# Kernel tuning notes

Measured on AMD Instinct MI355X. Metric: run time of the kernel, lower is better.

The kernel has to match this reference:

```python
import jax, jax.numpy as jnp
import numpy as np

B, C, L = 4, 256, 2048
HEADS, DIM_HEAD = 8, 64
HIDDEN = HEADS * DIM_HEAD  # 512


def setup_inputs() -> dict:
    key = jax.random.key(0)
    k1, k2, k3, k4 = jax.random.split(key, 4)
    x = jax.random.normal(k1, (B, C, L), dtype=jnp.float32)
    # Conv1d kernel_size=1 weights, squeezed to [out_ch, in_ch]
    w_qkv = jax.random.normal(k2, (3 * HIDDEN, C), dtype=jnp.float32) * (1.0 / np.sqrt(C))
    w_out = jax.random.normal(k3, (C, HIDDEN), dtype=jnp.float32) * (1.0 / np.sqrt(HIDDEN))
    b_out = jax.random.normal(k4, (C,), dtype=jnp.float32) * 0.01
    return {"x": x, "w_qkv": w_qkv, "w_out": w_out, "b_out": b_out}


def reference(x, w_qkv, w_out, b_out):
    b, c, l = x.shape
    scale = DIM_HEAD ** (-0.5)
    # pointwise conv == channel matmul
    qkv = jnp.einsum('oc,bcl->bol', w_qkv, x)  # [b, 3*hidden, l]
    q, k, v = jnp.split(qkv, 3, axis=1)        # each [b, hidden, l]
    def to_heads(t):
        return t.reshape(b, HEADS, DIM_HEAD, l)  # b h d l
    q, k, v = to_heads(q), to_heads(k), to_heads(v)
    q = q * scale
    sim = jnp.einsum('bhdi,bhdj->bhij', q, k)   # [b,h,l,l]
    attn = jax.nn.softmax(sim, axis=-1)          # stable softmax (max-subtract inside)
    out = jnp.einsum('bhij,bhdj->bhid', attn, v)  # [b,h,l,d]
    out = out.transpose(0, 1, 3, 2).reshape(b, HIDDEN, l)  # b (h d) l
    return jnp.einsum('oc,bcl->bol', w_out, out) + b_out[None, :, None]
```

## Files before the change

kernel.cpp:

```cpp
#include <hip/hip_runtime.h>

typedef unsigned short u16;
typedef unsigned int u32;
typedef __bf16 bf16x8 __attribute__((ext_vector_type(8)));
typedef float f32x4 __attribute__((ext_vector_type(4)));
typedef float f32x8 __attribute__((ext_vector_type(8)));
typedef float f32x16 __attribute__((ext_vector_type(16)));

#define MFMA16(a, b, c) __builtin_amdgcn_mfma_f32_16x16x32_bf16((a), (b), (c), 0, 0, 0)
#define MFMA32(a, b, c) __builtin_amdgcn_mfma_f32_32x32x16_bf16((a), (b), (c), 0, 0, 0)

#define Bn 4
#define Cn 256
#define Ln 2048
#define Hn 8
#define Dn 64
#define HID 512
#define SEGELEMS 4194304

__device__ __forceinline__ u16 bf16_rne(float f) {
  u32 u = __builtin_bit_cast(u32, f);
  u += 0x7FFFu + ((u >> 16) & 1u);
  return (u16)(u >> 16);
}

__device__ __forceinline__ unsigned pack2(float a, float b) {
  return (unsigned)bf16_rne(a) | ((unsigned)bf16_rne(b) << 16);
}

__device__ __forceinline__ float bf16_up(u16 v) {
  u32 u = ((u32)v) << 16;
  return __builtin_bit_cast(float, u);
}

__device__ __forceinline__ float fast_exp2(float x) {
#if __has_builtin(__builtin_amdgcn_exp2f)
  return __builtin_amdgcn_exp2f(x);
#else
  return exp2f(x);
#endif
}

__device__ __forceinline__ float fast_rcp(float x) {
#if __has_builtin(__builtin_amdgcn_rcpf)
  return __builtin_amdgcn_rcpf(x);
#else
  return 1.0f / x;
#endif
}

__device__ __forceinline__ void async_load16(const u16* g, u16* l) {
  __builtin_amdgcn_global_load_lds(
      (const __attribute__((address_space(1))) void*)g,
      (__attribute__((address_space(3))) void*)l, 16, 0, 0);
}

__global__ __launch_bounds__(256) void prep_all(const float* __restrict__ wqkv,
                                                const float* __restrict__ wout,
                                                const float* __restrict__ x,
                                                u16* __restrict__ wq,
                                                u16* __restrict__ wo,
                                                u16* __restrict__ xT) {
  const int t = threadIdx.x;
  if (blockIdx.x < 2048) {
    int i = blockIdx.x * 256 + t;
    const float QSCALE = 0.125f * 1.44269504088896340736f;
    if (i < 3 * HID * Cn) {
      float v = wqkv[i];
      if (i < HID * Cn) v *= QSCALE;
      wq[i] = bf16_rne(v);
    } else {
      int j = i - 3 * HID * Cn;
      wo[j] = bf16_rne(wout[j]);
    }
    return;
  }
  __shared__ u16 tile[64][72];
  int v = blockIdx.x - 2048;
  const int lt = v & 31, ct = (v >> 5) & 3, b = v >> 7;
  const float* xp = x + ((size_t)b * Cn + ct * 64) * Ln + lt * 64;
  for (int pass = 0; pass < 4; ++pass) {
    int c = pass * 16 + (t >> 4);
    int l4 = (t & 15) * 4;
    float4 vf = *(const float4*)(xp + (size_t)c * Ln + l4);
    tile[l4 + 0][c] = bf16_rne(vf.x);
    tile[l4 + 1][c] = bf16_rne(vf.y);
    tile[l4 + 2][c] = bf16_rne(vf.z);
    tile[l4 + 3][c] = bf16_rne(vf.w);
  }
  __syncthreads();
  u16* op = xT + ((size_t)b * Ln + lt * 64) * Cn + ct * 64;
  for (int pass = 0; pass < 2; ++pass) {
    int id = pass * 256 + t;
    int l = id >> 3, c8 = (id & 7) * 8;
    *(uint4*)(op + (size_t)l * Cn + c8) = *(const uint4*)&tile[l][c8];
  }
}

__global__ __launch_bounds__(256, 4) void qkv_gemm(const u16* __restrict__ wq,
                                                   const u16* __restrict__ xT,
                                                   u16* __restrict__ qT,
                                                   u16* __restrict__ kT,
                                                   u16* __restrict__ vv) {
  __shared__ u16 Bs[4096];
  __shared__ u16 Aq[4096];
  __shared__ u16 Ak[4096];
  __shared__ u16 Av[4096];
  const int t = threadIdx.x;
  const int nt = blockIdx.x, head = blockIdx.y, b = blockIdx.z;
  const int n0 = nt * 64, m0 = head * 64;
  const int w = t >> 6, lane = t & 63, q = lane >> 4, ln = lane & 15;

  const u16* Bg = xT + ((size_t)b * Ln + n0) * Cn;
  const u16* AgQ = wq + (size_t)m0 * Cn;
  const u16* AgK = wq + (size_t)(512 + m0) * Cn;
  const u16* AgV = wq + (size_t)(1024 + m0) * Cn;

  f32x4 zf = {0.f, 0.f, 0.f, 0.f};
  f32x4 accQ[4], accK[4], accV[4];
  for (int i = 0; i < 4; ++i) { accQ[i] = zf; accK[i] = zf; accV[i] = zf; }

  const int pr0 = w * 8 + (lane >> 3), pr1 = (4 + w) * 8 + (lane >> 3);
  const int pc0 = (lane & 7) ^ (pr0 & 7), pc1 = (lane & 7) ^ (pr1 & 7);

  for (int kk = 0; kk < 4; ++kk) {
    int k0 = kk * 64;
    async_load16(Bg + (size_t)pr0 * Cn + k0 + pc0 * 8, &Bs[w * 512]);
    async_load16(Bg + (size_t)pr1 * Cn + k0 + pc1 * 8, &Bs[(4 + w) * 512]);
    async_load16(AgQ + (size_t)pr0 * Cn + k0 + pc0 * 8, &Aq[w * 512]);
    async_load16(AgQ + (size_t)pr1 * Cn + k0 + pc1 * 8, &Aq[(4 + w) * 512]);
    async_load16(AgK + (size_t)pr0 * Cn + k0 + pc0 * 8, &Ak[w * 512]);
    async_load16(AgK + (size_t)pr1 * Cn + k0 + pc1 * 8, &Ak[(4 + w) * 512]);
    async_load16(AgV + (size_t)pr0 * Cn + k0 + pc0 * 8, &Av[w * 512]);
    async_load16(AgV + (size_t)pr1 * Cn + k0 + pc1 * 8, &Av[(4 + w) * 512]);
    __syncthreads();
    int ar = w * 16 + ln;
    bf16x8 aq0 = *(const bf16x8*)&Aq[ar * 64 + ((q ^ (ln & 7)) * 8)];
    bf16x8 aq1 = *(const bf16x8*)&Aq[ar * 64 + (((q + 4) ^ (ln & 7)) * 8)];
    bf16x8 ak0 = *(const bf16x8*)&Ak[ar * 64 + ((q ^ (ln & 7)) * 8)];
    bf16x8 ak1 = *(const bf16x8*)&Ak[ar * 64 + (((q + 4) ^ (ln & 7)) * 8)];
    bf16x8 av0 = *(const bf16x8*)&Av[ar * 64 + ((q ^ (ln & 7)) * 8)];
    bf16x8 av1 = *(const bf16x8*)&Av[ar * 64 + (((q + 4) ^ (ln & 7)) * 8)];
    for (int n2 = 0; n2 < 4; ++n2) {
      int br = n2 * 16 + ln;
      bf16x8 b0 = *(const bf16x8*)&Bs[br * 64 + ((q ^ (ln & 7)) * 8)];
      bf16x8 b1 = *(const bf16x8*)&Bs[br * 64 + (((q + 4) ^ (ln & 7)) * 8)];
      accQ[n2] = MFMA16(aq0, b0, accQ[n2]);
      accQ[n2] = MFMA16(aq1, b1, accQ[n2]);
      accK[n2] = MFMA16(ak0, b0, accK[n2]);
      accK[n2] = MFMA16(ak1, b1, accK[n2]);
      accV[n2] = MFMA16(av0, b0, accV[n2]);
      accV[n2] = MFMA16(av1, b1, accV[n2]);
    }
    __syncthreads();
  }

  int od0 = w * 16 + q * 4;
  int cw = od0 >> 3, lo = od0 & 7;
  for (int n2 = 0; n2 < 4; ++n2) {
    int l = n2 * 16 + ln;
    uint2 pk;
    pk.x = pack2(accQ[n2][0], accQ[n2][1]);
    pk.y = pack2(accQ[n2][2], accQ[n2][3]);
    *(uint2*)&Bs[l * 64 + ((cw ^ (l & 7)) * 8) + lo] = pk;
  }
  __syncthreads();
  {
    u16* dst = qT + (((size_t)b * Hn + head) * Ln + n0) * Dn;
    for (int pass = 0; pass < 2; ++pass) {
      int id = pass * 256 + t;
      int l = id >> 3, c = id & 7;
      *(uint4*)(dst + (size_t)l * Dn + c * 8) =
          *(const uint4*)&Bs[l * 64 + ((c ^ (l & 7)) * 8)];
    }
  }
  __syncthreads();
  for (int n2 = 0; n2 < 4; ++n2) {
    int l = n2 * 16 + ln;
    uint2 pk;
    pk.x = pack2(accK[n2][0], accK[n2][1]);
    pk.y = pack2(accK[n2][2], accK[n2][3]);
    *(uint2*)&Bs[l * 64 + ((cw ^ (l & 7)) * 8) + lo] = pk;
  }
  __syncthreads();
  {
    u16* dst = kT + (((size_t)b * Hn + head) * Ln + n0) * Dn;
    for (int pass = 0; pass < 2; ++pass) {
      int id = pass * 256 + t;
      int l = id >> 3, c = id & 7;
      *(uint4*)(dst + (size_t)l * Dn + c * 8) =
          *(const uint4*)&Bs[l * 64 + ((c ^ (l & 7)) * 8)];
    }
  }
  __syncthreads();
  for (int n2 = 0; n2 < 4; ++n2) {
    int l = n2 * 16 + ln;
    int lpm = (l & ~12) | ((l & 4) << 1) | ((l & 8) >> 1);
    int cl = lpm >> 3, lov = lpm & 7;
    for (int r = 0; r < 4; ++r) {
      int od = w * 16 + q * 4 + r;
      Bs[od * 64 + ((cl ^ (od & 7)) * 8) + lov] = bf16_rne(accV[n2][r]);
    }
  }
  __syncthreads();
  {
    u16* dst = vv + ((size_t)b * HID + head * 64) * Ln + n0;
    for (int pass = 0; pass < 2; ++pass) {
      int id = pass * 256 + t;
      int od = id >> 3, c = id & 7;
      *(uint4*)(dst + (size_t)od * Ln + c * 8) =
          *(const uint4*)&Bs[od * 64 + ((c ^ (od & 7)) * 8)];
    }
  }
}

__global__ __launch_bounds__(256, 4) void attention(const u16* __restrict__ qT,
                                                    const u16* __restrict__ kT,
                                                    const u16* __restrict__ vv,
                                                    u16* __restrict__ pO,
                                                    float* __restrict__ lP) {
  __shared__ u16 Kt[4096];
  __shared__ u16 Vt[4096];
  const int t = threadIdx.x;
  const int qb = blockIdx.x, bh = blockIdx.y, seg = blockIdx.z;
  const int b = bh >> 3, hh = bh & 7;
  const int w = t >> 6, lane = t & 63;
  const int li = lane & 31, h = lane >> 5;
  const int i0 = qb * 128 + w * 32;

  bf16x8 qf0, qf1, qf2, qf3;
  {
    const u16* qrow = qT + (((size_t)bh) * Ln + i0 + li) * Dn + h * 8;
    qf0 = *(const bf16x8*)(qrow + 0);
    qf1 = *(const bf16x8*)(qrow + 16);
    qf2 = *(const bf16x8*)(qrow + 32);
    qf3 = *(const bf16x8*)(qrow + 48);
  }

  const u16* ksrc0 = kT + ((size_t)bh) * Ln * Dn;
  const u16* vsrc0 = vv + ((size_t)b * HID + hh * Dn) * Ln;

  f32x16 z16;
#pragma unroll
  for (int r = 0; r < 16; ++r) z16[r] = 0.f;
  f32x16 o0 = z16, o1 = z16;
  float lp = 0.f;

  const int pr0 = w * 8 + (lane >> 3), pr1 = (4 + w) * 8 + (lane >> 3);
  const int pc0 = (lane & 7) ^ (pr0 & 7), pc1 = (lane & 7) ^ (pr1 & 7);
  const u16* kadr0 = ksrc0 + ((size_t)seg * 1024 + pr0) * Dn + pc0 * 8;
  const u16* kadr1 = ksrc0 + ((size_t)seg * 1024 + pr1) * Dn + pc1 * 8;
  const u16* vadr0 = vsrc0 + (size_t)pr0 * Ln + seg * 1024 + pc0 * 8;
  const u16* vadr1 = vsrc0 + (size_t)pr1 * Ln + seg * 1024 + pc1 * 8;

  const int sw = (li & 7);

  for (int jt = 0; jt < 16; ++jt) {
    int j0 = jt * 64;
    async_load16(kadr0 + (size_t)j0 * Dn, &Kt[w * 512]);
    async_load16(kadr1 + (size_t)j0 * Dn, &Kt[(4 + w) * 512]);
    async_load16(vadr0 + j0, &Vt[w * 512]);
    async_load16(vadr1 + j0, &Vt[(4 + w) * 512]);
    __syncthreads();

    f32x16 sv0, sv1;
    {
      bf16x8 k0 = *(const bf16x8*)&Kt[li * 64 + (((0 + h) ^ sw) * 8)];
      bf16x8 k1 = *(const bf16x8*)&Kt[(32 + li) * 64 + (((0 + h) ^ sw) * 8)];
      sv0 = MFMA32(k0, qf0, z16);
      sv1 = MFMA32(k1, qf0, z16);
    }
    {
      bf16x8 k0 = *(const bf16x8*)&Kt[li * 64 + (((2 + h) ^ sw) * 8)];
      bf16x8 k1 = *(const bf16x8*)&Kt[(32 + li) * 64 + (((2 + h) ^ sw) * 8)];
      sv0 = MFMA32(k0, qf1, sv0);
      sv1 = MFMA32(k1, qf1, sv1);
    }
    {
      bf16x8 k0 = *(const bf16x8*)&Kt[li * 64 + (((4 + h) ^ sw) * 8)];
      bf16x8 k1 = *(const bf16x8*)&Kt[(32 + li) * 64 + (((4 + h) ^ sw) * 8)];
      sv0 = MFMA32(k0, qf2, sv0);
      sv1 = MFMA32(k1, qf2, sv1);
    }
    {
      bf16x8 k0 = *(const bf16x8*)&Kt[li * 64 + (((6 + h) ^ sw) * 8)];
      bf16x8 k1 = *(const bf16x8*)&Kt[(32 + li) * 64 + (((6 + h) ^ sw) * 8)];
      sv0 = MFMA32(k0, qf3, sv0);
      sv1 = MFMA32(k1, qf3, sv1);
    }

#pragma unroll
    for (int g = 0; g < 16; ++g) {
      sv0[g] = fast_exp2(sv0[g]);
      sv1[g] = fast_exp2(sv1[g]);
      lp += sv0[g] + sv1[g];
    }
    f32x8 e0 = __builtin_shufflevector(sv0, sv0, 0, 1, 2, 3, 4, 5, 6, 7);
    f32x8 e1 = __builtin_shufflevector(sv0, sv0, 8, 9, 10, 11, 12, 13, 14, 15);
    f32x8 e2 = __builtin_shufflevector(sv1, sv1, 0, 1, 2, 3, 4, 5, 6, 7);
    f32x8 e3 = __builtin_shufflevector(sv1, sv1, 8, 9, 10, 11, 12, 13, 14, 15);
    bf16x8 pf0 = __builtin_convertvector(e0, bf16x8);
    bf16x8 pf1 = __builtin_convertvector(e1, bf16x8);
    bf16x8 pf2 = __builtin_convertvector(e2, bf16x8);
    bf16x8 pf3 = __builtin_convertvector(e3, bf16x8);

#pragma unroll
    for (int jc = 0; jc < 4; ++jc) {
      int ch = 2 * jc + h;
      bf16x8 pf = (jc == 0) ? pf0 : (jc == 1) ? pf1 : (jc == 2) ? pf2 : pf3;
      bf16x8 vf0 = *(const bf16x8*)&Vt[li * 64 + ((ch ^ sw) * 8)];
      bf16x8 vf1 = *(const bf16x8*)&Vt[(32 + li) * 64 + ((ch ^ sw) * 8)];
      o0 = MFMA32(pf, vf0, o0);
      o1 = MFMA32(pf, vf1, o1);
    }
    __syncthreads();
  }

  float lsum = lp + __shfl_xor(lp, 32);
  if (h == 0)
    lP[(((size_t)seg * Bn + b) * Hn + hh) * Ln + i0 + li] = lsum;
  u16* po = pO + (size_t)seg * SEGELEMS;
#pragma unroll
  for (int r = 0; r < 16; ++r) {
    int ir = (r & 3) + 8 * (r >> 2) + 4 * h;
    size_t base = ((size_t)b * Ln + i0 + ir) * HID + hh * Dn + li;
    po[base] = bf16_rne(o0[r]);
    po[base + 32] = bf16_rne(o1[r]);
  }
}

__global__ __launch_bounds__(256) void combine(const u16* __restrict__ pO,
                                               const float* __restrict__ lP,
                                               u16* __restrict__ attT) {
  int idx8 = (blockIdx.x * 256 + threadIdx.x) * 8;
  int i_lin = idx8 >> 9;
  int h = (idx8 & 511) >> 6;
  int b = i_lin >> 11, i = i_lin & 2047;
  float l = lP[(b * 8 + h) * 2048 + i] + lP[(32 + b * 8 + h) * 2048 + i];
  float s = fast_rcp(l);
  uint4 u0 = *(const uint4*)(pO + idx8);
  uint4 u1 = *(const uint4*)(pO + SEGELEMS + idx8);
  u32 a[4] = {u0.x, u0.y, u0.z, u0.w};
  u32 c[4] = {u1.x, u1.y, u1.z, u1.w};
  uint4 r;
  u32 rw[4];
#pragma unroll
  for (int k = 0; k < 4; ++k) {
    float flo = (bf16_up((u16)(a[k] & 0xFFFF)) + bf16_up((u16)(c[k] & 0xFFFF))) * s;
    float fhi = (bf16_up((u16)(a[k] >> 16)) + bf16_up((u16)(c[k] >> 16))) * s;
    rw[k] = pack2(flo, fhi);
  }
  r.x = rw[0]; r.y = rw[1]; r.z = rw[2]; r.w = rw[3];
  *(uint4*)(attT + idx8) = r;
}

__global__ __launch_bounds__(256, 4) void out_gemm(const u16* __restrict__ wo,
                                                   const u16* __restrict__ attT,
                                                   const float* __restrict__ bout,
                                                   float* __restrict__ out) {
  __shared__ u16 As[4096];
  __shared__ u16 Bs[2048];
  const int t = threadIdx.x;
  const int nt = blockIdx.x, mt = blockIdx.y, b = blockIdx.z;
  const int m0 = mt * 64, n0 = nt * 32;
  const int w = t >> 6, lane = t & 63, q = lane >> 4, ln = lane & 15;

  const u16* Ag = wo + (size_t)m0 * HID;
  const u16* Bg = attT + ((size_t)b * Ln + n0) * HID;

  f32x4 zf = {0.f, 0.f, 0.f, 0.f};
  f32x4 acc[2];
  acc[0] = zf; acc[1] = zf;

  const int pr0 = w * 8 + (lane >> 3), pr1 = (4 + w) * 8 + (lane >> 3);
  const int pc0 = (lane & 7) ^ (pr0 & 7), pc1 = (lane & 7) ^ (pr1 & 7);
  const u16* Aad0 = Ag + (size_t)pr0 * HID + pc0 * 8;
  const u16* Aad1 = Ag + (size_t)pr1 * HID + pc1 * 8;
  const u16* Bad0 = Bg + (size_t)pr0 * HID + pc0 * 8;

#define LOADAB(kk, A0, A1, B0)                   \
  {                                              \
    int k0_ = (kk) * 64;                         \
    A0 = *(const uint4*)(Aad0 + k0_);            \
    A1 = *(const uint4*)(Aad1 + k0_);            \
    B0 = *(const uint4*)(Bad0 + k0_);            \
  }
#define STOREAB(A0, A1, B0)                      \
  {                                              \
    *(uint4*)&As[w * 512 + lane * 8] = A0;       \
    *(uint4*)&As[(4 + w) * 512 + lane * 8] = A1; \
    *(uint4*)&Bs[w * 512 + lane * 8] = B0;       \
  }
#define COMPUTEC()                                                             \
  {                                                                            \
    int ar = w * 16 + ln;                                                      \
    bf16x8 a0 = *(const bf16x8*)&As[ar * 64 + ((q ^ (ln & 7)) * 8)];           \
    bf16x8 a1 = *(const bf16x8*)&As[ar * 64 + (((q + 4) ^ (ln & 7)) * 8)];     \
    for (int n2 = 0; n2 < 2; ++n2) {                                           \
      int br = n2 * 16 + ln;                                                   \
      bf16x8 b0 = *(const bf16x8*)&Bs[br * 64 + ((q ^ (ln & 7)) * 8)];         \
      bf16x8 b1 = *(const bf16x8*)&Bs[br * 64 + (((q + 4) ^ (ln & 7)) * 8)];   \
      acc[n2] = MFMA16(a0, b0, acc[n2]);                                       \
      acc[n2] = MFMA16(a1, b1, acc[n2]);                                       \
    }                                                                          \
  }

  uint4 aa0, aa1, ba0, ab0, ab1, bb0;
  LOADAB(0, aa0, aa1, ba0);
  for (int kk = 0; kk < 8; kk += 2) {
    if (kk) __syncthreads();
    STOREAB(aa0, aa1, ba0);
    __syncthreads();
    LOADAB(kk + 1, ab0, ab1, bb0);
    COMPUTEC();
    __syncthreads();
    STOREAB(ab0, ab1, bb0);
    __syncthreads();
    if (kk + 2 < 8) LOADAB(kk + 2, aa0, aa1, ba0);
    COMPUTEC();
  }
#undef LOADAB
#undef STOREAB
#undef COMPUTEC

  float bias[4];
  for (int r = 0; r < 4; ++r) bias[r] = bout[m0 + w * 16 + q * 4 + r];
  for (int n2 = 0; n2 < 2; ++n2) {
    int l = n0 + n2 * 16 + ln;
    for (int r = 0; r < 4; ++r) {
      int o = m0 + w * 16 + q * 4 + r;
      out[((size_t)b * Cn + o) * Ln + l] = acc[n2][r] + bias[r];
    }
  }
}

extern "C" void kernel_launch(void* const* d_in, const int* in_sizes, int n_in,
                              void* d_out, int out_size, void* d_ws, size_t ws_size,
                              hipStream_t stream) {
  const float* x = (const float*)d_in[0];
  const float* wqkv = (const float*)d_in[1];
  const float* wout = (const float*)d_in[2];
  const float* bout = (const float*)d_in[3];
  float* out = (float*)d_out;
  char* ws = (char*)d_ws;

  u16* wq_b  = (u16*)(ws + 0);
  u16* wo_b  = (u16*)(ws + 786432);
  float* lP  = (float*)(ws + 1048576);
  u16* qT    = (u16*)(ws + 1572864);
  u16* kT    = (u16*)(ws + 9961472);
  u16* vv    = (u16*)(ws + 18350080);
  u16* xT    = (u16*)(ws + 26738688);
  u16* pO    = (u16*)(ws + 26738688);
  u16* attT  = qT;

  prep_all<<<2560, 256, 0, stream>>>(wqkv, wout, x, wq_b, wo_b, xT);
  qkv_gemm<<<dim3(32, 8, 4), 256, 0, stream>>>(wq_b, xT, qT, kT, vv);
  attention<<<dim3(16, 32, 2), 256, 0, stream>>>(qT, kT, vv, pO, lP);
  combine<<<2048, 256, 0, stream>>>(pO, lP, attT);
  out_gemm<<<dim3(64, 4, 4), 256, 0, stream>>>(wo_b, attT, bout, out);
}
```

Before: 136.3 us.

## Fuse split-KV combine into output GEMM and register-prefetch K/V tiles

The separate combine kernel is removed. The output GEMM now loads both partial attention outputs and their row sums, normalizes them, and stages the result in shared memory. This saves a kernel launch and a full write and read of the intermediate attT tensor. In the attention loop, the async direct-to-LDS K/V loads are replaced with register double-buffered global loads followed by LDS stores, which costs more registers and changes the overlap pattern.

```diff
diff --git a/kernel.cpp b/kernel.cpp
--- a/kernel.cpp
+++ b/kernel.cpp
@@ -31,6 +31,12 @@
 __device__ __forceinline__ float bf16_up(u16 v) {
   u32 u = ((u32)v) << 16;
   return __builtin_bit_cast(float, u);
+}
+
+__device__ __forceinline__ u32 comb2(u32 a, u32 c, float s) {
+  float lo = (bf16_up((u16)(a & 0xFFFF)) + bf16_up((u16)(c & 0xFFFF))) * s;
+  float hi = (bf16_up((u16)(a >> 16)) + bf16_up((u16)(c >> 16))) * s;
+  return pack2(lo, hi);
 }
 
 __device__ __forceinline__ float fast_exp2(float x) {
@@ -255,66 +261,89 @@
 
   const int sw = (li & 7);
 
-  for (int jt = 0; jt < 16; ++jt) {
-    int j0 = jt * 64;
-    async_load16(kadr0 + (size_t)j0 * Dn, &Kt[w * 512]);
-    async_load16(kadr1 + (size_t)j0 * Dn, &Kt[(4 + w) * 512]);
-    async_load16(vadr0 + j0, &Vt[w * 512]);
-    async_load16(vadr1 + j0, &Vt[(4 + w) * 512]);
-    __syncthreads();
-
-    f32x16 sv0, sv1;
-    {
-      bf16x8 k0 = *(const bf16x8*)&Kt[li * 64 + (((0 + h) ^ sw) * 8)];
-      bf16x8 k1 = *(const bf16x8*)&Kt[(32 + li) * 64 + (((0 + h) ^ sw) * 8)];
-      sv0 = MFMA32(k0, qf0, z16);
-      sv1 = MFMA32(k1, qf0, z16);
-    }
-    {
-      bf16x8 k0 = *(const bf16x8*)&Kt[li * 64 + (((2 + h) ^ sw) * 8)];
-      bf16x8 k1 = *(const bf16x8*)&Kt[(32 + li) * 64 + (((2 + h) ^ sw) * 8)];
-      sv0 = MFMA32(k0, qf1, sv0);
-      sv1 = MFMA32(k1, qf1, sv1);
-    }
-    {
-      bf16x8 k0 = *(const bf16x8*)&Kt[li * 64 + (((4 + h) ^ sw) * 8)];
-      bf16x8 k1 = *(const bf16x8*)&Kt[(32 + li) * 64 + (((4 + h) ^ sw) * 8)];
-      sv0 = MFMA32(k0, qf2, sv0);
-      sv1 = MFMA32(k1, qf2, sv1);
-    }
-    {
-      bf16x8 k0 = *(const bf16x8*)&Kt[li * 64 + (((6 + h) ^ sw) * 8)];
-      bf16x8 k1 = *(const bf16x8*)&Kt[(32 + li) * 64 + (((6 + h) ^ sw) * 8)];
-      sv0 = MFMA32(k0, qf3, sv0);
-      sv1 = MFMA32(k1, qf3, sv1);
-    }
-
-#pragma unroll
-    for (int g = 0; g < 16; ++g) {
-      sv0[g] = fast_exp2(sv0[g]);
-      sv1[g] = fast_exp2(sv1[g]);
-      lp += sv0[g] + sv1[g];
-    }
-    f32x8 e0 = __builtin_shufflevector(sv0, sv0, 0, 1, 2, 3, 4, 5, 6, 7);
-    f32x8 e1 = __builtin_shufflevector(sv0, sv0, 8, 9, 10, 11, 12, 13, 14, 15);
-    f32x8 e2 = __builtin_shufflevector(sv1, sv1, 0, 1, 2, 3, 4, 5, 6, 7);
-    f32x8 e3 = __builtin_shufflevector(sv1, sv1, 8, 9, 10, 11, 12, 13, 14, 15);
-    bf16x8 pf0 = __builtin_convertvector(e0, bf16x8);
-    bf16x8 pf1 = __builtin_convertvector(e1, bf16x8);
-    bf16x8 pf2 = __builtin_convertvector(e2, bf16x8);
-    bf16x8 pf3 = __builtin_convertvector(e3, bf16x8);
-
-#pragma unroll
-    for (int jc = 0; jc < 4; ++jc) {
-      int ch = 2 * jc + h;
-      bf16x8 pf = (jc == 0) ? pf0 : (jc == 1) ? pf1 : (jc == 2) ? pf2 : pf3;
-      bf16x8 vf0 = *(const bf16x8*)&Vt[li * 64 + ((ch ^ sw) * 8)];
-      bf16x8 vf1 = *(const bf16x8*)&Vt[(32 + li) * 64 + ((ch ^ sw) * 8)];
-      o0 = MFMA32(pf, vf0, o0);
-      o1 = MFMA32(pf, vf1, o1);
-    }
-    __syncthreads();
-  }
+#define LOADKV(jt, K0, K1, V0, V1)                              \
+  {                                                             \
+    int j0_ = (jt) * 64;                                        \
+    K0 = *(const uint4*)(kadr0 + (size_t)j0_ * Dn);             \
+    K1 = *(const uint4*)(kadr1 + (size_t)j0_ * Dn);             \
+    V0 = *(const uint4*)(vadr0 + j0_);                          \
+    V1 = *(const uint4*)(vadr1 + j0_);                          \
+  }
+#define STOREKV(K0, K1, V0, V1)                                 \
+  {                                                             \
+    *(uint4*)&Kt[w * 512 + lane * 8] = K0;                      \
+    *(uint4*)&Kt[(4 + w) * 512 + lane * 8] = K1;                \
+    *(uint4*)&Vt[w * 512 + lane * 8] = V0;                      \
+    *(uint4*)&Vt[(4 + w) * 512 + lane * 8] = V1;                \
+  }
+
+#define COMPUTE()                                                              \
+  {                                                                            \
+    f32x16 sv0, sv1;                                                           \
+    {                                                                          \
+      bf16x8 k0 = *(const bf16x8*)&Kt[li * 64 + (((0 + h) ^ sw) * 8)];         \
+      bf16x8 k1 = *(const bf16x8*)&Kt[(32 + li) * 64 + (((0 + h) ^ sw) * 8)];  \
+      sv0 = MFMA32(k0, qf0, z16);                                              \
+      sv1 = MFMA32(k1, qf0, z16);                                              \
+    }                                                                          \
+    {                                                                          \
+      bf16x8 k0 = *(const bf16x8*)&Kt[li * 64 + (((2 + h) ^ sw) * 8)];         \
+      bf16x8 k1 = *(const bf16x8*)&Kt[(32 + li) * 64 + (((2 + h) ^ sw) * 8)];  \
+      sv0 = MFMA32(k0, qf1, sv0);                                              \
+      sv1 = MFMA32(k1, qf1, sv1);                                              \
+    }                                                                          \
+    {                                                                          \
+      bf16x8 k0 = *(const bf16x8*)&Kt[li * 64 + (((4 + h) ^ sw) * 8)];         \
+      bf16x8 k1 = *(const bf16x8*)&Kt[(32 + li) * 64 + (((4 + h) ^ sw) * 8)];  \
+      sv0 = MFMA32(k0, qf2, sv0);                                              \
+      sv1 = MFMA32(k1, qf2, sv1);                                              \
+    }                                                                          \
+    {                                                                          \
+      bf16x8 k0 = *(const bf16x8*)&Kt[li * 64 + (((6 + h) ^ sw) * 8)];         \
+      bf16x8 k1 = *(const bf16x8*)&Kt[(32 + li) * 64 + (((6 + h) ^ sw) * 8)];  \
+      sv0 = MFMA32(k0, qf3, sv0);                                              \
+      sv1 = MFMA32(k1, qf3, sv1);                                              \
+    }                                                                          \
+    _Pragma("unroll") for (int g = 0; g < 16; ++g) {                           \
+      sv0[g] = fast_exp2(sv0[g]);                                              \
+      sv1[g] = fast_exp2(sv1[g]);                                              \
+      lp += sv0[g] + sv1[g];                                                   \
+    }                                                                          \
+    f32x8 e0 = __builtin_shufflevector(sv0, sv0, 0, 1, 2, 3, 4, 5, 6, 7);      \
+    f32x8 e1 = __builtin_shufflevector(sv0, sv0, 8, 9, 10, 11, 12, 13, 14, 15);\
+    f32x8 e2 = __builtin_shufflevector(sv1, sv1, 0, 1, 2, 3, 4, 5, 6, 7);      \
+    f32x8 e3 = __builtin_shufflevector(sv1, sv1, 8, 9, 10, 11, 12, 13, 14, 15);\
+    bf16x8 pf0 = __builtin_convertvector(e0, bf16x8);                          \
+    bf16x8 pf1 = __builtin_convertvector(e1, bf16x8);                          \
+    bf16x8 pf2 = __builtin_convertvector(e2, bf16x8);                          \
+    bf16x8 pf3 = __builtin_convertvector(e3, bf16x8);                          \
+    _Pragma("unroll") for (int jc = 0; jc < 4; ++jc) {                         \
+      int ch = 2 * jc + h;                                                     \
+      bf16x8 pf = (jc == 0) ? pf0 : (jc == 1) ? pf1 : (jc == 2) ? pf2 : pf3;   \
+      bf16x8 vf0 = *(const bf16x8*)&Vt[li * 64 + ((ch ^ sw) * 8)];             \
+      bf16x8 vf1 = *(const bf16x8*)&Vt[(32 + li) * 64 + ((ch ^ sw) * 8)];      \
+      o0 = MFMA32(pf, vf0, o0);                                                \
+      o1 = MFMA32(pf, vf1, o1);                                                \
+    }                                                                          \
+  }
+
+  uint4 ka0, ka1, va0, va1, kb0, kb1, vb0, vb1;
+  LOADKV(0, ka0, ka1, va0, va1);
+  for (int jt = 0; jt < 16; jt += 2) {
+    if (jt) __syncthreads();
+    STOREKV(ka0, ka1, va0, va1);
+    __syncthreads();
+    LOADKV(jt + 1, kb0, kb1, vb0, vb1);
+    COMPUTE();
+    __syncthreads();
+    STOREKV(kb0, kb1, vb0, vb1);
+    __syncthreads();
+    if (jt + 2 < 16) LOADKV(jt + 2, ka0, ka1, va0, va1);
+    COMPUTE();
+  }
+#undef LOADKV
+#undef STOREKV
+#undef COMPUTE
 
   float lsum = lp + __shfl_xor(lp, 32);
   if (h == 0)
@@ -329,33 +358,9 @@
   }
 }
 
-__global__ __launch_bounds__(256) void combine(const u16* __restrict__ pO,
-                                               const float* __restrict__ lP,
-                                               u16* __restrict__ attT) {
-  int idx8 = (blockIdx.x * 256 + threadIdx.x) * 8;
-  int i_lin = idx8 >> 9;
-  int h = (idx8 & 511) >> 6;
-  int b = i_lin >> 11, i = i_lin & 2047;
-  float l = lP[(b * 8 + h) * 2048 + i] + lP[(32 + b * 8 + h) * 2048 + i];
-  float s = fast_rcp(l);
-  uint4 u0 = *(const uint4*)(pO + idx8);
-  uint4 u1 = *(const uint4*)(pO + SEGELEMS + idx8);
-  u32 a[4] = {u0.x, u0.y, u0.z, u0.w};
-  u32 c[4] = {u1.x, u1.y, u1.z, u1.w};
-  uint4 r;
-  u32 rw[4];
-#pragma unroll
-  for (int k = 0; k < 4; ++k) {
-    float flo = (bf16_up((u16)(a[k] & 0xFFFF)) + bf16_up((u16)(c[k] & 0xFFFF))) * s;
-    float fhi = (bf16_up((u16)(a[k] >> 16)) + bf16_up((u16)(c[k] >> 16))) * s;
-    rw[k] = pack2(flo, fhi);
-  }
-  r.x = rw[0]; r.y = rw[1]; r.z = rw[2]; r.w = rw[3];
-  *(uint4*)(attT + idx8) = r;
-}
-
 __global__ __launch_bounds__(256, 4) void out_gemm(const u16* __restrict__ wo,
-                                                   const u16* __restrict__ attT,
+                                                   const u16* __restrict__ pO,
+                                                   const float* __restrict__ lP,
                                                    const float* __restrict__ bout,
                                                    float* __restrict__ out) {
   __shared__ u16 As[4096];
@@ -366,7 +371,6 @@
   const int w = t >> 6, lane = t & 63, q = lane >> 4, ln = lane & 15;
 
   const u16* Ag = wo + (size_t)m0 * HID;
-  const u16* Bg = attT + ((size_t)b * Ln + n0) * HID;
 
   f32x4 zf = {0.f, 0.f, 0.f, 0.f};
   f32x4 acc[2];
@@ -376,20 +380,33 @@
   const int pc0 = (lane & 7) ^ (pr0 & 7), pc1 = (lane & 7) ^ (pr1 & 7);
   const u16* Aad0 = Ag + (size_t)pr0 * HID + pc0 * 8;
   const u16* Aad1 = Ag + (size_t)pr1 * HID + pc1 * 8;
-  const u16* Bad0 = Bg + (size_t)pr0 * HID + pc0 * 8;
-
-#define LOADAB(kk, A0, A1, B0)                   \
+  const int irow = n0 + pr0;
+  const u16* Bs0 = pO + ((size_t)b * Ln + irow) * HID + pc0 * 8;
+  const u16* Bs1 = Bs0 + SEGELEMS;
+  const float* lp0 = lP + (size_t)b * Hn * Ln + irow;
+  const float* lp1 = lP + (size_t)(Bn + b) * Hn * Ln + irow;
+
+#define LOADAB(kk, A0, A1, U0, U1, L0, L1)       \
   {                                              \
     int k0_ = (kk) * 64;                         \
     A0 = *(const uint4*)(Aad0 + k0_);            \
     A1 = *(const uint4*)(Aad1 + k0_);            \
-    B0 = *(const uint4*)(Bad0 + k0_);            \
-  }
-#define STOREAB(A0, A1, B0)                      \
+    U0 = *(const uint4*)(Bs0 + k0_);             \
+    U1 = *(const uint4*)(Bs1 + k0_);             \
+    L0 = lp0[(size_t)(kk) * Ln];                 \
+    L1 = lp1[(size_t)(kk) * Ln];                 \
+  }
+#define STOREAB(A0, A1, U0, U1, L0, L1)          \
   {                                              \
+    float s_ = fast_rcp(L0 + L1);                \
+    uint4 Bc_;                                   \
+    Bc_.x = comb2(U0.x, U1.x, s_);               \
+    Bc_.y = comb2(U0.y, U1.y, s_);               \
+    Bc_.z = comb2(U0.z, U1.z, s_);               \
+    Bc_.w = comb2(U0.w, U1.w, s_);               \
     *(uint4*)&As[w * 512 + lane * 8] = A0;       \
     *(uint4*)&As[(4 + w) * 512 + lane * 8] = A1; \
-    *(uint4*)&Bs[w * 512 + lane * 8] = B0;       \
+    *(uint4*)&Bs[w * 512 + lane * 8] = Bc_;      \
   }
 #define COMPUTEC()                                                             \
   {                                                                            \
@@ -405,18 +422,19 @@
     }                                                                          \
   }
 
-  uint4 aa0, aa1, ba0, ab0, ab1, bb0;
-  LOADAB(0, aa0, aa1, ba0);
+  uint4 aa0, aa1, ua0, ua1, ab0, ab1, ub0, ub1;
+  float la0, la1, lb0, lb1;
+  LOADAB(0, aa0, aa1, ua0, ua1, la0, la1);
   for (int kk = 0; kk < 8; kk += 2) {
     if (kk) __syncthreads();
-    STOREAB(aa0, aa1, ba0);
-    __syncthreads();
-    LOADAB(kk + 1, ab0, ab1, bb0);
+    STOREAB(aa0, aa1, ua0, ua1, la0, la1);
+    __syncthreads();
+    LOADAB(kk + 1, ab0, ab1, ub0, ub1, lb0, lb1);
     COMPUTEC();
     __syncthreads();
-    STOREAB(ab0, ab1, bb0);
-    __syncthreads();
-    if (kk + 2 < 8) LOADAB(kk + 2, aa0, aa1, ba0);
+    STOREAB(ab0, ab1, ub0, ub1, lb0, lb1);
+    __syncthreads();
+    if (kk + 2 < 8) LOADAB(kk + 2, aa0, aa1, ua0, ua1, la0, la1);
     COMPUTEC();
   }
 #undef LOADAB
@@ -452,11 +470,9 @@
   u16* vv    = (u16*)(ws + 18350080);
   u16* xT    = (u16*)(ws + 26738688);
   u16* pO    = (u16*)(ws + 26738688);
-  u16* attT  = qT;
 
   prep_all<<<2560, 256, 0, stream>>>(wqkv, wout, x, wq_b, wo_b, xT);
   qkv_gemm<<<dim3(32, 8, 4), 256, 0, stream>>>(wq_b, xT, qT, kT, vv);
   attention<<<dim3(16, 32, 2), 256, 0, stream>>>(qT, kT, vv, pO, lP);
-  combine<<<2048, 256, 0, stream>>>(pO, lP, attT);
-  out_gemm<<<dim3(64, 4, 4), 256, 0, stream>>>(wo_b, attT, bout, out);
-}
+  out_gemm<<<dim3(64, 4, 4), 256, 0, stream>>>(wo_b, pO, lP, bout, out);
+}
```

Result: slower. 164.3 us (+20.6%).

## Fuse split-K combine into out_gemm and give attention waves two query tiles

Applied to the files above, without the earlier changes.

The separate combine kernel is removed. out_gemm now loads both partial attention outputs and their row sums, normalises them and writes the combined bf16 tile into shared memory before the MFMA loop, which saves one launch and one global round trip of the attention tensor. The attention kernel moves to 128-thread blocks in which each wave handles 64 query rows (two 32-row tiles), so every K/V fragment read from LDS feeds twice as many MFMAs. In exchange, register pressure per wave rises and each block has half as many waves to hide latency.

```diff
diff --git a/kernel.cpp b/kernel.cpp
--- a/kernel.cpp
+++ b/kernel.cpp
@@ -31,6 +31,12 @@
 __device__ __forceinline__ float bf16_up(u16 v) {
   u32 u = ((u32)v) << 16;
   return __builtin_bit_cast(float, u);
+}
+
+__device__ __forceinline__ u32 comb2(u32 a, u32 c, float s) {
+  float lo = (bf16_up((u16)(a & 0xFFFF)) + bf16_up((u16)(c & 0xFFFF))) * s;
+  float hi = (bf16_up((u16)(a >> 16)) + bf16_up((u16)(c >> 16))) * s;
+  return pack2(lo, hi);
 }
 
 __device__ __forceinline__ float fast_exp2(float x) {
@@ -214,7 +220,7 @@
   }
 }
 
-__global__ __launch_bounds__(256, 4) void attention(const u16* __restrict__ qT,
+__global__ __launch_bounds__(128, 2) void attention(const u16* __restrict__ qT,
                                                     const u16* __restrict__ kT,
                                                     const u16* __restrict__ vv,
                                                     u16* __restrict__ pO,
@@ -226,15 +232,20 @@
   const int b = bh >> 3, hh = bh & 7;
   const int w = t >> 6, lane = t & 63;
   const int li = lane & 31, h = lane >> 5;
-  const int i0 = qb * 128 + w * 32;
-
-  bf16x8 qf0, qf1, qf2, qf3;
+  const int i0 = qb * 128 + w * 64;
+
+  bf16x8 qA0, qA1, qA2, qA3, qB0, qB1, qB2, qB3;
   {
-    const u16* qrow = qT + (((size_t)bh) * Ln + i0 + li) * Dn + h * 8;
-    qf0 = *(const bf16x8*)(qrow + 0);
-    qf1 = *(const bf16x8*)(qrow + 16);
-    qf2 = *(const bf16x8*)(qrow + 32);
-    qf3 = *(const bf16x8*)(qrow + 48);
+    const u16* qra = qT + (((size_t)bh) * Ln + i0 + li) * Dn + h * 8;
+    const u16* qrb = qT + (((size_t)bh) * Ln + i0 + 32 + li) * Dn + h * 8;
+    qA0 = *(const bf16x8*)(qra + 0);
+    qA1 = *(const bf16x8*)(qra + 16);
+    qA2 = *(const bf16x8*)(qra + 32);
+    qA3 = *(const bf16x8*)(qra + 48);
+    qB0 = *(const bf16x8*)(qrb + 0);
+    qB1 = *(const bf16x8*)(qrb + 16);
+    qB2 = *(const bf16x8*)(qrb + 32);
+    qB3 = *(const bf16x8*)(qrb + 48);
   }
 
   const u16* ksrc0 = kT + ((size_t)bh) * Ln * Dn;
@@ -243,119 +254,136 @@
   f32x16 z16;
 #pragma unroll
   for (int r = 0; r < 16; ++r) z16[r] = 0.f;
-  f32x16 o0 = z16, o1 = z16;
-  float lp = 0.f;
-
-  const int pr0 = w * 8 + (lane >> 3), pr1 = (4 + w) * 8 + (lane >> 3);
-  const int pc0 = (lane & 7) ^ (pr0 & 7), pc1 = (lane & 7) ^ (pr1 & 7);
-  const u16* kadr0 = ksrc0 + ((size_t)seg * 1024 + pr0) * Dn + pc0 * 8;
-  const u16* kadr1 = ksrc0 + ((size_t)seg * 1024 + pr1) * Dn + pc1 * 8;
-  const u16* vadr0 = vsrc0 + (size_t)pr0 * Ln + seg * 1024 + pc0 * 8;
-  const u16* vadr1 = vsrc0 + (size_t)pr1 * Ln + seg * 1024 + pc1 * 8;
-
-  const int sw = (li & 7);
+  f32x16 oA0 = z16, oA1 = z16, oB0 = z16, oB1 = z16;
+  float lpA = 0.f, lpB = 0.f;
+
+  const int sr0 = (0 * 2 + w) * 8 + (lane >> 3);
+  const int sr1 = (1 * 2 + w) * 8 + (lane >> 3);
+  const int sr2 = (2 * 2 + w) * 8 + (lane >> 3);
+  const int sr3 = (3 * 2 + w) * 8 + (lane >> 3);
+  const int sc0 = (lane & 7) ^ (sr0 & 7), sc1 = (lane & 7) ^ (sr1 & 7);
+  const int sc2 = (lane & 7) ^ (sr2 & 7), sc3 = (lane & 7) ^ (sr3 & 7);
+  const u16* ka0 = ksrc0 + ((size_t)seg * 1024 + sr0) * Dn + sc0 * 8;
+  const u16* ka1 = ksrc0 + ((size_t)seg * 1024 + sr1) * Dn + sc1 * 8;
+  const u16* ka2 = ksrc0 + ((size_t)seg * 1024 + sr2) * Dn + sc2 * 8;
+  const u16* ka3 = ksrc0 + ((size_t)seg * 1024 + sr3) * Dn + sc3 * 8;
+  const u16* va0 = vsrc0 + (size_t)sr0 * Ln + seg * 1024 + sc0 * 8;
+  const u16* va1 = vsrc0 + (size_t)sr1 * Ln + seg * 1024 + sc1 * 8;
+  const u16* va2 = vsrc0 + (size_t)sr2 * Ln + seg * 1024 + sc2 * 8;
+  const u16* va3 = vsrc0 + (size_t)sr3 * Ln + seg * 1024 + sc3 * 8;
+
+  const int sw = li & 7;
 
   for (int jt = 0; jt < 16; ++jt) {
     int j0 = jt * 64;
-    async_load16(kadr0 + (size_t)j0 * Dn, &Kt[w * 512]);
-    async_load16(kadr1 + (size_t)j0 * Dn, &Kt[(4 + w) * 512]);
-    async_load16(vadr0 + j0, &Vt[w * 512]);
-    async_load16(vadr1 + j0, &Vt[(4 + w) * 512]);
-    __syncthreads();
-
-    f32x16 sv0, sv1;
+    async_load16(ka0 + (size_t)j0 * Dn, &Kt[(0 * 2 + w) * 512]);
+    async_load16(ka1 + (size_t)j0 * Dn, &Kt[(1 * 2 + w) * 512]);
+    async_load16(ka2 + (size_t)j0 * Dn, &Kt[(2 * 2 + w) * 512]);
+    async_load16(ka3 + (size_t)j0 * Dn, &Kt[(3 * 2 + w) * 512]);
+    async_load16(va0 + j0, &Vt[(0 * 2 + w) * 512]);
+    async_load16(va1 + j0, &Vt[(1 * 2 + w) * 512]);
+    async_load16(va2 + j0, &Vt[(2 * 2 + w) * 512]);
+    async_load16(va3 + j0, &Vt[(3 * 2 + w) * 512]);
+    __syncthreads();
+
+    f32x16 svA0, svA1, svB0, svB1;
     {
       bf16x8 k0 = *(const bf16x8*)&Kt[li * 64 + (((0 + h) ^ sw) * 8)];
       bf16x8 k1 = *(const bf16x8*)&Kt[(32 + li) * 64 + (((0 + h) ^ sw) * 8)];
-      sv0 = MFMA32(k0, qf0, z16);
-      sv1 = MFMA32(k1, qf0, z16);
+      svA0 = MFMA32(k0, qA0, z16);
+      svA1 = MFMA32(k1, qA0, z16);
+      svB0 = MFMA32(k0, qB0, z16);
+      svB1 = MFMA32(k1, qB0, z16);
     }
     {
       bf16x8 k0 = *(const bf16x8*)&Kt[li * 64 + (((2 + h) ^ sw) * 8)];
       bf16x8 k1 = *(const bf16x8*)&Kt[(32 + li) * 64 + (((2 + h) ^ sw) * 8)];
-      sv0 = MFMA32(k0, qf1, sv0);
-      sv1 = MFMA32(k1, qf1, sv1);
+      svA0 = MFMA32(k0, qA1, svA0);
+      svA1 = MFMA32(k1, qA1, svA1);
+      svB0 = MFMA32(k0, qB1, svB0);
+      svB1 = MFMA32(k1, qB1, svB1);
     }
     {
       bf16x8 k0 = *(const bf16x8*)&Kt[li * 64 + (((4 + h) ^ sw) * 8)];
       bf16x8 k1 = *(const bf16x8*)&Kt[(32 + li) * 64 + (((4 + h) ^ sw) * 8)];
-      sv0 = MFMA32(k0, qf2, sv0);
-      sv1 = MFMA32(k1, qf2, sv1);
+      svA0 = MFMA32(k0, qA2, svA0);
+      svA1 = MFMA32(k1, qA2, svA1);
+      svB0 = MFMA32(k0, qB2, svB0);
+      svB1 = MFMA32(k1, qB2, svB1);
     }
     {
       bf16x8 k0 = *(const bf16x8*)&Kt[li * 64 + (((6 + h) ^ sw) * 8)];
       bf16x8 k1 = *(const bf16x8*)&Kt[(32 + li) * 64 + (((6 + h) ^ sw) * 8)];
-      sv0 = MFMA32(k0, qf3, sv0);
-      sv1 = MFMA32(k1, qf3, sv1);
+      svA0 = MFMA32(k0, qA3, svA0);
+      svA1 = MFMA32(k1, qA3, svA1);
+      svB0 = MFMA32(k0, qB3, svB0);
+      svB1 = MFMA32(k1, qB3, svB1);
     }
 
 #pragma unroll
     for (int g = 0; g < 16; ++g) {
-      sv0[g] = fast_exp2(sv0[g]);
-      sv1[g] = fast_exp2(sv1[g]);
-      lp += sv0[g] + sv1[g];
-    }
-    f32x8 e0 = __builtin_shufflevector(sv0, sv0, 0, 1, 2, 3, 4, 5, 6, 7);
-    f32x8 e1 = __builtin_shufflevector(sv0, sv0, 8, 9, 10, 11, 12, 13, 14, 15);
-    f32x8 e2 = __builtin_shufflevector(sv1, sv1, 0, 1, 2, 3, 4, 5, 6, 7);
-    f32x8 e3 = __builtin_shufflevector(sv1, sv1, 8, 9, 10, 11, 12, 13, 14, 15);
-    bf16x8 pf0 = __builtin_convertvector(e0, bf16x8);
-    bf16x8 pf1 = __builtin_convertvector(e1, bf16x8);
-    bf16x8 pf2 = __builtin_convertvector(e2, bf16x8);
-    bf16x8 pf3 = __builtin_convertvector(e3, bf16x8);
+      svA0[g] = fast_exp2(svA0[g]);
+      svA1[g] = fast_exp2(svA1[g]);
+      lpA += svA0[g] + svA1[g];
+      svB0[g] = fast_exp2(svB0[g]);
+      svB1[g] = fast_exp2(svB1[g]);
+      lpB += svB0[g] + svB1[g];
+    }
+    bf16x8 pfA0 = __builtin_convertvector(
+        __builtin_shufflevector(svA0, svA0, 0, 1, 2, 3, 4, 5, 6, 7), bf16x8);
+    bf16x8 pfA1 = __builtin_convertvector(
+        __builtin_shufflevector(svA0, svA0, 8, 9, 10, 11, 12, 13, 14, 15), bf16x8);
+    bf16x8 pfA2 = __builtin_convertvector(
+        __builtin_shufflevector(svA1, svA1, 0, 1, 2, 3, 4, 5, 6, 7), bf16x8);
+    bf16x8 pfA3 = __builtin_convertvector(
+        __builtin_shufflevector(svA1, svA1, 8, 9, 10, 11, 12, 13, 14, 15), bf16x8);
+    bf16x8 pfB0 = __builtin_convertvector(
+        __builtin_shufflevector(svB0, svB0, 0, 1, 2, 3, 4, 5, 6, 7), bf16x8);
+    bf16x8 pfB1 = __builtin_convertvector(
+        __builtin_shufflevector(svB0, svB0, 8, 9, 10, 11, 12, 13, 14, 15), bf16x8);
+    bf16x8 pfB2 = __builtin_convertvector(
+        __builtin_shufflevector(svB1, svB1, 0, 1, 2, 3, 4, 5, 6, 7), bf16x8);
+    bf16x8 pfB3 = __builtin_convertvector(
+        __builtin_shufflevector(svB1, svB1, 8, 9, 10, 11, 12, 13, 14, 15), bf16x8);
 
 #pragma unroll
     for (int jc = 0; jc < 4; ++jc) {
       int ch = 2 * jc + h;
-      bf16x8 pf = (jc == 0) ? pf0 : (jc == 1) ? pf1 : (jc == 2) ? pf2 : pf3;
+      bf16x8 pa = (jc == 0) ? pfA0 : (jc == 1) ? pfA1 : (jc == 2) ? pfA2 : pfA3;
+      bf16x8 pb = (jc == 0) ? pfB0 : (jc == 1) ? pfB1 : (jc == 2) ? pfB2 : pfB3;
       bf16x8 vf0 = *(const bf16x8*)&Vt[li * 64 + ((ch ^ sw) * 8)];
       bf16x8 vf1 = *(const bf16x8*)&Vt[(32 + li) * 64 + ((ch ^ sw) * 8)];
-      o0 = MFMA32(pf, vf0, o0);
-      o1 = MFMA32(pf, vf1, o1);
-    }
-    __syncthreads();
-  }
-
-  float lsum = lp + __shfl_xor(lp, 32);
-  if (h == 0)
-    lP[(((size_t)seg * Bn + b) * Hn + hh) * Ln + i0 + li] = lsum;
+      oA0 = MFMA32(pa, vf0, oA0);
+      oA1 = MFMA32(pa, vf1, oA1);
+      oB0 = MFMA32(pb, vf0, oB0);
+      oB1 = MFMA32(pb, vf1, oB1);
+    }
+    __syncthreads();
+  }
+
+  float lsA = lpA + __shfl_xor(lpA, 32);
+  float lsB = lpB + __shfl_xor(lpB, 32);
+  if (h == 0) {
+    size_t lbase = (((size_t)seg * Bn + b) * Hn + hh) * Ln + i0 + li;
+    lP[lbase] = lsA;
+    lP[lbase + 32] = lsB;
+  }
   u16* po = pO + (size_t)seg * SEGELEMS;
 #pragma unroll
   for (int r = 0; r < 16; ++r) {
     int ir = (r & 3) + 8 * (r >> 2) + 4 * h;
-    size_t base = ((size_t)b * Ln + i0 + ir) * HID + hh * Dn + li;
-    po[base] = bf16_rne(o0[r]);
-    po[base + 32] = bf16_rne(o1[r]);
-  }
-}
-
-__global__ __launch_bounds__(256) void combine(const u16* __restrict__ pO,
-                                               const float* __restrict__ lP,
-                                               u16* __restrict__ attT) {
-  int idx8 = (blockIdx.x * 256 + threadIdx.x) * 8;
-  int i_lin = idx8 >> 9;
-  int h = (idx8 & 511) >> 6;
-  int b = i_lin >> 11, i = i_lin & 2047;
-  float l = lP[(b * 8 + h) * 2048 + i] + lP[(32 + b * 8 + h) * 2048 + i];
-  float s = fast_rcp(l);
-  uint4 u0 = *(const uint4*)(pO + idx8);
-  uint4 u1 = *(const uint4*)(pO + SEGELEMS + idx8);
-  u32 a[4] = {u0.x, u0.y, u0.z, u0.w};
-  u32 c[4] = {u1.x, u1.y, u1.z, u1.w};
-  uint4 r;
-  u32 rw[4];
-#pragma unroll
-  for (int k = 0; k < 4; ++k) {
-    float flo = (bf16_up((u16)(a[k] & 0xFFFF)) + bf16_up((u16)(c[k] & 0xFFFF))) * s;
-    float fhi = (bf16_up((u16)(a[k] >> 16)) + bf16_up((u16)(c[k] >> 16))) * s;
-    rw[k] = pack2(flo, fhi);
-  }
-  r.x = rw[0]; r.y = rw[1]; r.z = rw[2]; r.w = rw[3];
-  *(uint4*)(attT + idx8) = r;
+    size_t baseA = ((size_t)b * Ln + i0 + ir) * HID + hh * Dn + li;
+    po[baseA] = bf16_rne(oA0[r]);
+    po[baseA + 32] = bf16_rne(oA1[r]);
+    size_t baseB = ((size_t)b * Ln + i0 + 32 + ir) * HID + hh * Dn + li;
+    po[baseB] = bf16_rne(oB0[r]);
+    po[baseB + 32] = bf16_rne(oB1[r]);
+  }
 }
 
 __global__ __launch_bounds__(256, 4) void out_gemm(const u16* __restrict__ wo,
-                                                   const u16* __restrict__ attT,
+                                                   const u16* __restrict__ pO,
+                                                   const float* __restrict__ lP,
                                                    const float* __restrict__ bout,
                                                    float* __restrict__ out) {
   __shared__ u16 As[4096];
@@ -366,7 +394,6 @@
   const int w = t >> 6, lane = t & 63, q = lane >> 4, ln = lane & 15;
 
   const u16* Ag = wo + (size_t)m0 * HID;
-  const u16* Bg = attT + ((size_t)b * Ln + n0) * HID;
 
   f32x4 zf = {0.f, 0.f, 0.f, 0.f};
   f32x4 acc[2];
@@ -376,20 +403,33 @@
   const int pc0 = (lane & 7) ^ (pr0 & 7), pc1 = (lane & 7) ^ (pr1 & 7);
   const u16* Aad0 = Ag + (size_t)pr0 * HID + pc0 * 8;
   const u16* Aad1 = Ag + (size_t)pr1 * HID + pc1 * 8;
-  const u16* Bad0 = Bg + (size_t)pr0 * HID + pc0 * 8;
-
-#define LOADAB(kk, A0, A1, B0)                   \
+  const int irow = n0 + pr0;
+  const u16* Bs0 = pO + ((size_t)b * Ln + irow) * HID + pc0 * 8;
+  const u16* Bs1 = Bs0 + SEGELEMS;
+  const float* lp0 = lP + (size_t)b * Hn * Ln + irow;
+  const float* lp1 = lP + (size_t)(Bn + b) * Hn * Ln + irow;
+
+#define LOADAB(kk, A0, A1, U0, U1, L0, L1)       \
   {                                              \
     int k0_ = (kk) * 64;                         \
     A0 = *(const uint4*)(Aad0 + k0_);            \
     A1 = *(const uint4*)(Aad1 + k0_);            \
-    B0 = *(const uint4*)(Bad0 + k0_);            \
-  }
-#define STOREAB(A0, A1, B0)                      \
+    U0 = *(const uint4*)(Bs0 + k0_);             \
+    U1 = *(const uint4*)(Bs1 + k0_);             \
+    L0 = lp0[(size_t)(kk) * Ln];                 \
+    L1 = lp1[(size_t)(kk) * Ln];                 \
+  }
+#define STOREAB(A0, A1, U0, U1, L0, L1)          \
   {                                              \
+    float s_ = fast_rcp(L0 + L1);                \
+    uint4 Bc_;                                   \
+    Bc_.x = comb2(U0.x, U1.x, s_);               \
+    Bc_.y = comb2(U0.y, U1.y, s_);               \
+    Bc_.z = comb2(U0.z, U1.z, s_);               \
+    Bc_.w = comb2(U0.w, U1.w, s_);               \
     *(uint4*)&As[w * 512 + lane * 8] = A0;       \
     *(uint4*)&As[(4 + w) * 512 + lane * 8] = A1; \
-    *(uint4*)&Bs[w * 512 + lane * 8] = B0;       \
+    *(uint4*)&Bs[w * 512 + lane * 8] = Bc_;      \
   }
 #define COMPUTEC()                                                             \
   {                                                                            \
@@ -405,18 +445,19 @@
     }                                                                          \
   }
 
-  uint4 aa0, aa1, ba0, ab0, ab1, bb0;
-  LOADAB(0, aa0, aa1, ba0);
+  uint4 aa0, aa1, ua0, ua1, ab0, ab1, ub0, ub1;
+  float la0, la1, lb0, lb1;
+  LOADAB(0, aa0, aa1, ua0, ua1, la0, la1);
   for (int kk = 0; kk < 8; kk += 2) {
     if (kk) __syncthreads();
-    STOREAB(aa0, aa1, ba0);
-    __syncthreads();
-    LOADAB(kk + 1, ab0, ab1, bb0);
+    STOREAB(aa0, aa1, ua0, ua1, la0, la1);
+    __syncthreads();
+    LOADAB(kk + 1, ab0, ab1, ub0, ub1, lb0, lb1);
     COMPUTEC();
     __syncthreads();
-    STOREAB(ab0, ab1, bb0);
-    __syncthreads();
-    if (kk + 2 < 8) LOADAB(kk + 2, aa0, aa1, ba0);
+    STOREAB(ab0, ab1, ub0, ub1, lb0, lb1);
+    __syncthreads();
+    if (kk + 2 < 8) LOADAB(kk + 2, aa0, aa1, ua0, ua1, la0, la1);
     COMPUTEC();
   }
 #undef LOADAB
@@ -452,11 +493,9 @@
   u16* vv    = (u16*)(ws + 18350080);
   u16* xT    = (u16*)(ws + 26738688);
   u16* pO    = (u16*)(ws + 26738688);
-  u16* attT  = qT;
 
   prep_all<<<2560, 256, 0, stream>>>(wqkv, wout, x, wq_b, wo_b, xT);
   qkv_gemm<<<dim3(32, 8, 4), 256, 0, stream>>>(wq_b, xT, qT, kT, vv);
-  attention<<<dim3(16, 32, 2), 256, 0, stream>>>(qT, kT, vv, pO, lP);
-  combine<<<2048, 256, 0, stream>>>(pO, lP, attT);
-  out_gemm<<<dim3(64, 4, 4), 256, 0, stream>>>(wo_b, attT, bout, out);
-}
+  attention<<<dim3(16, 32, 2), 128, 0, stream>>>(qT, kT, vv, pO, lP);
+  out_gemm<<<dim3(64, 4, 4), 256, 0, stream>>>(wo_b, pO, lP, bout, out);
+}
```

New measurement: 135.4 us. No clear change (-0.7%).
